# Kernel optimization log

Hardware: AMD Instinct MI355X
Metric: run time of the kernel (lower is better)

The kernel has to match this reference:

```python
import jax, jax.numpy as jnp
import numpy as np

N_NODES = 100000
N_EDGES = 1600000
C = 64       # in_channels == filters
K = 3        # Chebyshev order
EPS = 1e-5   # InstanceNorm eps


def setup_inputs() -> dict:
    key = jax.random.key(0)
    ks = jax.random.split(key, 8)
    x = jax.random.normal(ks[0], (N_NODES, C), dtype=jnp.float32)
    edge_index = jax.random.randint(ks[1], (2, N_EDGES), 0, N_NODES, dtype=jnp.int64)
    scale = 1.0 / np.sqrt(C)
    W1 = jax.random.normal(ks[2], (K, C, C), dtype=jnp.float32) * scale
    b1 = jnp.zeros((C,), dtype=jnp.float32)
    W2 = jax.random.normal(ks[3], (K, C, C), dtype=jnp.float32) * scale
    b2 = jnp.zeros((C,), dtype=jnp.float32)
    return {"x": x, "edge_index": edge_index, "W1": W1, "b1": b1, "W2": W2, "b2": b2}


def _cheb_conv(x, src, dst, w_edge, W, b, n):
    # PyG ChebConv, norm='sym', lambda_max=2: L_hat = -D^{-1/2} A D^{-1/2}
    def prop(h):  # h: [N, C] -> L_hat @ h via gather -> weight -> scatter-add
        return jax.ops.segment_sum(w_edge[:, None] * h[src], dst, num_segments=n)
    Tx0 = x
    Tx1 = prop(x)
    Tx2 = 2.0 * prop(Tx1) - Tx0
    return Tx0 @ W[0] + Tx1 @ W[1] + Tx2 @ W[2] + b


def _instance_norm(h):
    # PyG InstanceNorm (single graph, affine=False): normalize over nodes per channel
    m = h.mean(axis=0, keepdims=True)
    v = h.var(axis=0, keepdims=True)
    return (h - m) * jax.lax.rsqrt(v + EPS)


def reference(x, edge_index, W1, b1, W2, b2):
    n = x.shape[0]
    src, dst = edge_index[0], edge_index[1]
    ones = jnp.ones((src.shape[0],), dtype=x.dtype)
    deg = jax.ops.segment_sum(ones, dst, num_segments=n)
    safe = jnp.where(deg > 0, deg, 1.0)
    dinv = jnp.where(deg > 0, jax.lax.rsqrt(safe), 0.0)
    w_edge = -dinv[src] * dinv[dst]  # scaled-Laplacian edge weights
    h = _instance_norm(jax.nn.relu(_cheb_conv(x, src, dst, w_edge, W1, b1, n)))
    h = _instance_norm(jax.nn.relu(_cheb_conv(h, src, dst, w_edge, W2, b2, n)))
    return h
```

## Files before the change

### kernel.cpp

```cpp
#include <hip/hip_runtime.h>
#include <hip/hip_fp16.h>

#define NCH 64
#define EPS 1e-5f
#define SBANKS 32
#define BSHIFT 8
#define NHIST 256
#define BINCAP 6400
#define PADRES 2048
#define RSHIFT 14
#define SRCMASK 0x1FFFFu
#define QW_SCALE 32767.0f
#define QW_INV (1.0f/32767.0f)

typedef _Float16 f16x8 __attribute__((ext_vector_type(8)));
typedef float f32x4 __attribute__((ext_vector_type(4)));

__global__ __launch_bounds__(256) void k_front(const float* __restrict__ x, __half* __restrict__ xh,
                                               int castTotal, int castB,
                                               const float* __restrict__ W1, _Float16* __restrict__ Wb1,
                                               const float* __restrict__ W2, _Float16* __restrict__ Wb2,
                                               const int* __restrict__ dst, int* __restrict__ cnt,
                                               int E, int per, int nbuck) {
    int bid = blockIdx.x;
    if (bid < castB) {
        int i = (bid * 256 + threadIdx.x) * 4;
        if (i < castTotal) {
            float4 f = *(const float4*)(x + i);
            __half2* o = (__half2*)(xh + i);
            o[0] = __floats2half2_rn(f.x, f.y);
            o[1] = __floats2half2_rn(f.z, f.w);
        }
        return;
    }
    if (bid < castB + 96) {
        int wb = bid - castB;
        const float* W = (wb < 48) ? W1 : W2;
        _Float16* Wb = (wb < 48) ? Wb1 : Wb2;
        int idx = (wb % 48) * 256 + threadIdx.x;
        int j = idx & 7;
        int lane = (idx >> 3) & 63;
        int tk = idx >> 9;
        int tile = tk / 6, kk = tk % 6;
        int k = kk * 32 + (lane >> 4) * 8 + j;
        int n = tile * 16 + (lane & 15);
        Wb[idx] = (_Float16)W[k * 64 + n];
        return;
    }
    __shared__ int lh[512];
    int hb = bid - castB - 96;
    for (int t = threadIdx.x; t < nbuck; t += 256) lh[t] = 0;
    __syncthreads();
    int lo = hb * per, hi = min(E, lo + per);
    for (int e = lo + threadIdx.x; e < hi; e += 256)
        atomicAdd(&lh[dst[e] >> BSHIFT], 1);
    __syncthreads();
    for (int t = threadIdx.x; t < nbuck; t += 256)
        if (lh[t]) atomicAdd(&cnt[t], lh[t]);
}

__global__ void k_bscan(const int* __restrict__ cnt, int* __restrict__ gbase,
                        int* __restrict__ gcur, int nbuck, int E) {
    __shared__ int s[512];
    int t = threadIdx.x;
    int v = (t < nbuck) ? cnt[t] : 0;
    s[t] = v;
    __syncthreads();
    for (int off = 1; off < 512; off <<= 1) {
        int add = (t >= off) ? s[t - off] : 0;
        __syncthreads();
        s[t] += add;
        __syncthreads();
    }
    if (t < nbuck) { int ex = s[t] - v; gbase[t] = ex; gcur[t] = ex; }
    if (t == 0) gbase[nbuck] = E;
}

__global__ __launch_bounds__(256) void k_bin(const int* __restrict__ src,
                                             const int* __restrict__ dst,
                                             int* __restrict__ gcur,
                                             int2* __restrict__ binned, int E, int per, int nbuck) {
    __shared__ int lh[512];
    __shared__ int lsc[512];
    __shared__ int lbase[512];
    __shared__ int lcur[512];
    __shared__ int2 sedge[BINCAP];
    int t = threadIdx.x;
    for (int i = t; i < 512; i += 256) lh[i] = 0;
    __syncthreads();
    int lo = blockIdx.x * per, hi = min(E, lo + per);
    for (int e = lo + t; e < hi; e += 256)
        atomicAdd(&lh[dst[e] >> BSHIFT], 1);
    __syncthreads();
    int v0 = lh[t], v1 = lh[t + 256];
    lsc[t] = v0; lsc[t + 256] = v1;
    __syncthreads();
    for (int off = 1; off < 512; off <<= 1) {
        int a0 = (t >= off) ? lsc[t - off] : 0;
        int a1 = (t + 256 >= off) ? lsc[t + 256 - off] : 0;
        __syncthreads();
        lsc[t] += a0; lsc[t + 256] += a1;
        __syncthreads();
    }
    lsc[t] -= v0; lsc[t + 256] -= v1;
    if (t < nbuck && v0) lbase[t] = atomicAdd(&gcur[t], v0);
    if (t + 256 < nbuck && v1) lbase[t + 256] = atomicAdd(&gcur[t + 256], v1);
    lcur[t] = lsc[t]; lcur[t + 256] = lsc[t + 256];
    __syncthreads();
    for (int e = lo + t; e < hi; e += 256) {
        int d = dst[e];
        int b = d >> BSHIFT;
        int pos = atomicAdd(&lcur[b], 1);
        sedge[pos] = make_int2(src[e], d);
    }
    __syncthreads();
    int cntE = hi - lo;
    for (int i = t; i < cntE; i += 256) {
        int2 sd = sedge[i];
        int b = sd.y >> BSHIFT;
        binned[lbase[b] + (i - lsc[b])] = sd;
    }
}

__global__ __launch_bounds__(256) void k_bucket(const int2* __restrict__ binned,
                                                const int* __restrict__ gbase,
                                                float* __restrict__ dinv,
                                                int2* __restrict__ rowinfo,
                                                unsigned int* __restrict__ csr, int N, int nbuck) {
    __shared__ int hist8[256 * 8];
    __shared__ int cur8[256 * 8];
    __shared__ int ldeg[256];
    __shared__ int ltmp[256];
    int b = blockIdx.x;
    int t = threadIdx.x;
    int nodeLo = b << BSHIFT;
    int nHere = min(256, N - nodeLo);
    int e0 = gbase[b], e1 = gbase[b + 1];
    int pb = (gbase[b] + b * PADRES + 7) & ~7;
    for (int i = t; i < 256 * 8; i += 256) hist8[i] = 0;
    __syncthreads();
    for (int e = e0 + t; e < e1; e += 256) {
        int2 sd = binned[e];
        atomicAdd(&hist8[((sd.y - nodeLo) << 3) + (sd.x >> RSHIFT)], 1);
    }
    __syncthreads();
    int c[8], deg = 0;
#pragma unroll
    for (int r = 0; r < 8; r++) { c[r] = hist8[(t << 3) + r]; deg += c[r]; }
    int pdeg = (deg + 7) & ~7;
    ldeg[t] = deg;
    if (t < nHere) dinv[nodeLo + t] = (deg > 0) ? rsqrtf((float)deg) : 0.0f;
    ltmp[t] = pdeg;
    __syncthreads();
    for (int off = 1; off < 256; off <<= 1) {
        int add = (t >= off) ? ltmp[t - off] : 0;
        __syncthreads();
        ltmp[t] += add;
        __syncthreads();
    }
    int lstart = ltmp[t] - pdeg;
    if (t < nHere) rowinfo[nodeLo + t] = make_int2(pb + lstart, pdeg);
    int run = lstart;
#pragma unroll
    for (int r = 0; r < 8; r++) { cur8[(t << 3) + r] = run; run += c[r]; }
    __syncthreads();
    for (int e = e0 + t; e < e1; e += 256) {
        int2 sd = binned[e];
        int dl = sd.y - nodeLo;
        int pos = atomicAdd(&cur8[(dl << 3) + (sd.x >> RSHIFT)], 1);
        unsigned int dd = (unsigned int)min(ldeg[dl], 32767);
        csr[pb + pos] = (unsigned int)sd.x | (dd << 17);
    }
    __syncthreads();
    if (t < nHere) {
        int d = ldeg[t];
        int pd = (d + 7) & ~7;
        if (pd > d) {
            unsigned int fill = (d > 0) ? (csr[pb + lstart] & SRCMASK) : 0u;
            for (int i = d; i < pd; i++) csr[pb + lstart + i] = fill;
        }
    }
}

__global__ void k_weights(unsigned int* __restrict__ csr, const float* __restrict__ dinv, int PE) {
    int e = blockIdx.x * blockDim.x + threadIdx.x;
    if (e < PE) {
        unsigned int v = csr[e];
        unsigned int d = v >> 17;
        if (d == 0) return;
        unsigned int s = v & SRCMASK;
        float aw = dinv[s] * rsqrtf((float)d);
        unsigned int qw = (unsigned int)(aw * QW_SCALE + 0.5f);
        csr[e] = s | (qw << 17);
    }
}


#define GATH(A0,A1,A2,A3,A4,A5,A6,A7, C0, C1) \
    A0 = *(const uint4*)(hb + (size_t)(C0.x & SRCMASK) * NCH); \
    A1 = *(const uint4*)(hb + (size_t)(C0.y & SRCMASK) * NCH); \
    A2 = *(const uint4*)(hb + (size_t)(C0.z & SRCMASK) * NCH); \
    A3 = *(const uint4*)(hb + (size_t)(C0.w & SRCMASK) * NCH); \
    A4 = *(const uint4*)(hb + (size_t)(C1.x & SRCMASK) * NCH); \
    A5 = *(const uint4*)(hb + (size_t)(C1.y & SRCMASK) * NCH); \
    A6 = *(const uint4*)(hb + (size_t)(C1.z & SRCMASK) * NCH); \
    A7 = *(const uint4*)(hb + (size_t)(C1.w & SRCMASK) * NCH);

#define FMA1(A, W) { \
    float2 f; \
    f = __half22float2(*(const __half2*)&A.x); acc[0] = fmaf(W, f.x, acc[0]); acc[1] = fmaf(W, f.y, acc[1]); \
    f = __half22float2(*(const __half2*)&A.y); acc[2] = fmaf(W, f.x, acc[2]); acc[3] = fmaf(W, f.y, acc[3]); \
    f = __half22float2(*(const __half2*)&A.z); acc[4] = fmaf(W, f.x, acc[4]); acc[5] = fmaf(W, f.y, acc[5]); \
    f = __half22float2(*(const __half2*)&A.w); acc[6] = fmaf(W, f.x, acc[6]); acc[7] = fmaf(W, f.y, acc[7]); }

#define FMA8(A0,A1,A2,A3,A4,A5,A6,A7, C0, C1) { \
    float w0 = -(float)(C0.x >> 17) * QW_INV; \
    float w1 = -(float)(C0.y >> 17) * QW_INV; \
    float w2 = -(float)(C0.z >> 17) * QW_INV; \
    float w3 = -(float)(C0.w >> 17) * QW_INV; \
    float w4 = -(float)(C1.x >> 17) * QW_INV; \
    float w5 = -(float)(C1.y >> 17) * QW_INV; \
    float w6 = -(float)(C1.z >> 17) * QW_INV; \
    float w7 = -(float)(C1.w >> 17) * QW_INV; \
    sw += ((w0 + w1) + (w2 + w3)) + ((w4 + w5) + (w6 + w7)); \
    FMA1(A0, w0) FMA1(A1, w1) FMA1(A2, w2) FMA1(A3, w3) \
    FMA1(A4, w4) FMA1(A5, w5) FMA1(A6, w6) FMA1(A7, w7) }

__global__ __launch_bounds__(256) void k_prop(const __half* __restrict__ h,
                                              const int2* __restrict__ rowinfo,
                                              const unsigned int* __restrict__ csr,
                                              const __half* __restrict__ tx0,
                                              __half* __restrict__ y, int N,
                                              const float* __restrict__ gstats,
                                              const float* __restrict__ tstats) {
    int lane = threadIdx.x & 63;
    int wv = (blockIdx.x * 256 + threadIdx.x) >> 6;
    int g = lane >> 3, li = lane & 7;
    int node = wv * 8 + g;
    int e = 0, eN = 0;
    if (node < N) {
        int2 info = rowinfo[node];
        e = info.x;
        eN = info.x + info.y;
    }
    float acc[8] = {0.f, 0.f, 0.f, 0.f, 0.f, 0.f, 0.f, 0.f};
    float sw = 0.0f;
    const __half* hb = h + li * 8;
    uint4 c0, c1, d0, d1;
    uint4 a0, a1, a2, a3, a4, a5, a6, a7;
    uint4 b0, b1, b2, b3, b4, b5, b6, b7;
    if (e < eN) {
        c0 = *(const uint4*)(csr + e);
        c1 = *(const uint4*)(csr + e + 4);
        int en = (e + 8 < eN) ? e + 8 : e;
        d0 = *(const uint4*)(csr + en);
        d1 = *(const uint4*)(csr + en + 4);
        GATH(a0, a1, a2, a3, a4, a5, a6, a7, c0, c1);
    }
    while (e + 8 < eN) {
        GATH(b0, b1, b2, b3, b4, b5, b6, b7, d0, d1);
        bool hasT = (e + 16 < eN);
        int enT = hasT ? e + 16 : e;
        uint4 t0 = *(const uint4*)(csr + enT);
        uint4 t1 = *(const uint4*)(csr + enT + 4);
        FMA8(a0, a1, a2, a3, a4, a5, a6, a7, c0, c1);
        if (hasT) { GATH(a0, a1, a2, a3, a4, a5, a6, a7, t0, t1); }
        int enD = (e + 24 < eN) ? e + 24 : e;
        uint4 u0 = *(const uint4*)(csr + enD);
        uint4 u1 = *(const uint4*)(csr + enD + 4);
        FMA8(b0, b1, b2, b3, b4, b5, b6, b7, d0, d1);
        c0 = t0; c1 = t1; d0 = u0; d1 = u1;
        e += 16;
    }
    if (e < eN) { FMA8(a0, a1, a2, a3, a4, a5, a6, a7, c0, c1); }
    if (node >= N) return;
    if (gstats != nullptr) {
        float4 m0 = *(const float4*)(gstats + li * 8);
        float4 m1 = *(const float4*)(gstats + li * 8 + 4);
        float4 r0 = *(const float4*)(gstats + 64 + li * 8);
        float4 r1 = *(const float4*)(gstats + 64 + li * 8 + 4);
        acc[0] = r0.x * (acc[0] - m0.x * sw);
        acc[1] = r0.y * (acc[1] - m0.y * sw);
        acc[2] = r0.z * (acc[2] - m0.z * sw);
        acc[3] = r0.w * (acc[3] - m0.w * sw);
        acc[4] = r1.x * (acc[4] - m1.x * sw);
        acc[5] = r1.y * (acc[5] - m1.y * sw);
        acc[6] = r1.z * (acc[6] - m1.z * sw);
        acc[7] = r1.w * (acc[7] - m1.w * sw);
    }
    if (tx0 != nullptr) {
        uint4 tq = *(const uint4*)(tx0 + (size_t)node * NCH + li * 8);
        float tv[8];
        float2 f;
        f = __half22float2(*(__half2*)&tq.x); tv[0] = f.x; tv[1] = f.y;
        f = __half22float2(*(__half2*)&tq.y); tv[2] = f.x; tv[3] = f.y;
        f = __half22float2(*(__half2*)&tq.z); tv[4] = f.x; tv[5] = f.y;
        f = __half22float2(*(__half2*)&tq.w); tv[6] = f.x; tv[7] = f.y;
        if (tstats != nullptr) {
            float4 m0 = *(const float4*)(tstats + li * 8);
            float4 m1 = *(const float4*)(tstats + li * 8 + 4);
            float4 r0 = *(const float4*)(tstats + 64 + li * 8);
            float4 r1 = *(const float4*)(tstats + 64 + li * 8 + 4);
            tv[0] = (tv[0] - m0.x) * r0.x; tv[1] = (tv[1] - m0.y) * r0.y;
            tv[2] = (tv[2] - m0.z) * r0.z; tv[3] = (tv[3] - m0.w) * r0.w;
            tv[4] = (tv[4] - m1.x) * r1.x; tv[5] = (tv[5] - m1.y) * r1.y;
            tv[6] = (tv[6] - m1.z) * r1.z; tv[7] = (tv[7] - m1.w) * r1.w;
        }
#pragma unroll
        for (int j = 0; j < 8; j++) acc[j] = 2.0f * acc[j] - tv[j];
    }
    uint4 o;
    __half2 hh;
    hh = __floats2half2_rn(acc[0], acc[1]); o.x = *(unsigned int*)&hh;
    hh = __floats2half2_rn(acc[2], acc[3]); o.y = *(unsigned int*)&hh;
    hh = __floats2half2_rn(acc[4], acc[5]); o.z = *(unsigned int*)&hh;
    hh = __floats2half2_rn(acc[6], acc[7]); o.w = *(unsigned int*)&hh;
    *(uint4*)(y + (size_t)node * NCH + li * 8) = o;
}

template <typename TOUT>
__global__ __launch_bounds__(256) void k_dmm(const __half* __restrict__ tx0,
                                             const __half* __restrict__ tx1,
                                             const __half* __restrict__ tx2,
                                             const _Float16* __restrict__ Wb,
                                             const float* __restrict__ b,
                                             TOUT* __restrict__ out,
                                             float* __restrict__ statsP, int N,
                                             const float* __restrict__ tstats) {
    __shared__ float sred[64];
    __shared__ float sq[64];
    int t = threadIdx.x;
    int w = t >> 6;
    int lane = t & 63;
    if (t < 64) { sred[t] = 0.f; sq[t] = 0.f; }
    __syncthreads();

    int nb16 = blockIdx.x * 64 + w * 16;
    int m = lane & 15, q = lane >> 4;
    int row = nb16 + m;
    int rowC = (row < N) ? row : 0;
    const __half* base0 = tx0 + (size_t)rowC * NCH;
    const __half* base1 = tx1 + (size_t)rowC * NCH;
    const __half* base2 = tx2 + (size_t)rowC * NCH;

    f32x4 acc[4];
#pragma unroll
    for (int tile = 0; tile < 4; tile++) acc[tile] = (f32x4){0.f, 0.f, 0.f, 0.f};

#pragma unroll
    for (int kk = 0; kk < 6; kk++) {
        const __half* ap = (kk < 2 ? base0 : (kk < 4 ? base1 : base2)) + (kk & 1) * 32 + q * 8;
        f16x8 a = *(const f16x8*)ap;
        if (kk < 2 && tstats != nullptr) {
            int cbase = (kk & 1) * 32 + q * 8;
#pragma unroll
            for (int j = 0; j < 8; j++) {
                float v = (float)a[j];
                a[j] = (_Float16)((v - tstats[cbase + j]) * tstats[64 + cbase + j]);
            }
        }
#pragma unroll
        for (int tile = 0; tile < 4; tile++) {
            f16x8 bf = *(const f16x8*)(Wb + ((size_t)(tile * 6 + kk) * 64 + lane) * 8);
            acc[tile] = __builtin_amdgcn_mfma_f32_16x16x32_f16(a, bf, acc[tile], 0, 0, 0);
        }
    }

#pragma unroll
    for (int tile = 0; tile < 4; tile++) {
        int ch = tile * 16 + m;
        float bb = b[ch];
        float s = 0.f, qq = 0.f;
#pragma unroll
        for (int r = 0; r < 4; r++) {
            int node = nb16 + q * 4 + r;
            float v = fmaxf(acc[tile][r] + bb, 0.f);
            if (node < N) {
                out[(size_t)node * NCH + ch] = (TOUT)v;
                s += v;
                qq = fmaf(v, v, qq);
            }
        }
        s += __shfl_xor(s, 16, 64);  s += __shfl_xor(s, 32, 64);
        qq += __shfl_xor(qq, 16, 64); qq += __shfl_xor(qq, 32, 64);
        if (q == 0) { atomicAdd(&sred[ch], s); atomicAdd(&sq[ch], qq); }
    }
    __syncthreads();
    if (t < 64) {
        int bank = blockIdx.x & (SBANKS - 1);
        atomicAdd(&statsP[bank * 128 + t], sred[t]);
        atomicAdd(&statsP[bank * 128 + 64 + t], sq[t]);
    }
}

__global__ void k_final(float* __restrict__ statsP, float invN) {
    int c = threadIdx.x;
    float S = 0.f, Q = 0.f;
    for (int k = 0; k < SBANKS; k++) {
        S += statsP[k * 128 + c];
        Q += statsP[k * 128 + 64 + c];
    }
    float m = S * invN;
    float var = Q * invN - m * m;
    statsP[SBANKS * 128 + c] = m;
    statsP[SBANKS * 128 + 64 + c] = rsqrtf(var + EPS);
}

__global__ void k_norm_hf(const __half* __restrict__ a, float* __restrict__ o,
                          const float* __restrict__ statsP, int total) {
    int i = blockIdx.x * blockDim.x + threadIdx.x;
    if (i >= total) return;
    int lane = i & 63;
    o[i] = (__half2float(a[i]) - statsP[SBANKS * 128 + lane]) * statsP[SBANKS * 128 + 64 + lane];
}

extern "C" void kernel_launch(void* const* d_in, const int* in_sizes, int n_in,
                              void* d_out, int out_size, void* d_ws, size_t ws_size,
                              hipStream_t stream) {
    const float* x  = (const float*)d_in[0];
    const int*   ei = (const int*)d_in[1];
    const float* W1 = (const float*)d_in[2];
    const float* b1 = (const float*)d_in[3];
    const float* W2 = (const float*)d_in[4];
    const float* b2 = (const float*)d_in[5];
    float* out = (float*)d_out;

    const int N = in_sizes[0] / NCH;
    const int E = in_sizes[1] / 2;
    const int* src = ei;
    const int* dst = ei + E;
    const int nbuck = (N + 255) >> BSHIFT;
    const int PE = E + nbuck * PADRES + 8;

    char* p = (char*)d_ws;
    auto alloc = [&](size_t bytes) {
        void* r = (void*)p;
        p += ((bytes + 255) / 256) * 256;
        return r;
    };
    float*  dinv     = (float*)alloc((size_t)131072 * 4);
    int2*   rowinfo  = (int2*)alloc((size_t)N * 8);
    unsigned int* csr = (unsigned int*)alloc((size_t)PE * 4);
    __half* xh       = (__half*)alloc((size_t)N * NCH * 2);
    __half* Tx1      = (__half*)alloc((size_t)N * NCH * 2);
    __half* Tx2      = (__half*)alloc((size_t)N * NCH * 2);
    __half* A        = (__half*)alloc((size_t)N * NCH * 2);
    __half* A2       = (__half*)alloc((size_t)N * NCH * 2);
    _Float16* Wb1    = (_Float16*)alloc(12288 * 2);
    _Float16* Wb2    = (_Float16*)alloc(12288 * 2);
    int*    gbase    = (int*)alloc((size_t)(nbuck + 1) * 4);
    int*    gcur     = (int*)alloc((size_t)nbuck * 4);
    const int statsFloats = SBANKS * 128 + 128;
    int*    cnt      = (int*)alloc((size_t)nbuck * 4 + (size_t)2 * statsFloats * 4);
    float*  stats1   = (float*)(cnt + nbuck);
    float*  stats2   = stats1 + statsFloats;
    const float* nrm1 = stats1 + SBANKS * 128;

    int2* binned = (int2*)Tx1;

    hipMemsetAsync(cnt, 0, (size_t)nbuck * 4 + (size_t)2 * statsFloats * 4, stream);

    const int TB = 256;
    int nbin = (E + BINCAP - 1) / BINCAP;
    if (nbin < 256) nbin = 256;
    const int perBin = (E + nbin - 1) / nbin;
    const int perH = (E + NHIST - 1) / NHIST;
    const int castTotal = N * NCH;
    const int castB = (castTotal / 4 + TB - 1) / TB;
    k_front<<<castB + 96 + NHIST, TB, 0, stream>>>(x, xh, castTotal, castB,
                                                   W1, Wb1, W2, Wb2,
                                                   dst, cnt, E, perH, nbuck);
    k_bscan<<<1, 512, 0, stream>>>(cnt, gbase, gcur, nbuck, E);
    k_bin<<<nbin, TB, 0, stream>>>(src, dst, gcur, binned, E, perBin, nbuck);
    k_bucket<<<nbuck, TB, 0, stream>>>(binned, gbase, dinv, rowinfo, csr, N, nbuck);
    k_weights<<<(PE + TB - 1) / TB, TB, 0, stream>>>(csr, dinv, PE);

    const int propWaves = (N + 7) / 8;
    const int propBlocks = (propWaves + 3) / 4;
    const int dmmBlocks = (N + 63) / 64;
    const int normBlocks = (N * NCH + TB - 1) / TB;
    const float invN = 1.0f / (float)N;

    k_prop<<<propBlocks, TB, 0, stream>>>(xh, rowinfo, csr, nullptr, Tx1, N, nullptr, nullptr);
    k_prop<<<propBlocks, TB, 0, stream>>>(Tx1, rowinfo, csr, xh, Tx2, N, nullptr, nullptr);
    k_dmm<__half><<<dmmBlocks, TB, 0, stream>>>(xh, Tx1, Tx2, Wb1, b1, A, stats1, N, nullptr);
    k_final<<<1, 64, 0, stream>>>(stats1, invN);

    k_prop<<<propBlocks, TB, 0, stream>>>(A, rowinfo, csr, nullptr, Tx1, N, nrm1, nullptr);
    k_prop<<<propBlocks, TB, 0, stream>>>(Tx1, rowinfo, csr, A, Tx2, N, nullptr, nrm1);
    k_dmm<__half><<<dmmBlocks, TB, 0, stream>>>(A, Tx1, Tx2, Wb2, b2, A2, stats2, N, nrm1);
    k_final<<<1, 64, 0, stream>>>(stats2, invN);
    k_norm_hf<<<normBlocks, TB, 0, stream>>>(A2, out, stats2, N * NCH);
}
```

Before: 341.7 us.

## Sort nodes by padded degree class to balance SpMM waves, simplify gather loop

Adds a degree-class histogram in k_bucket and a new k_perm kernel that builds a permutation grouping nodes by padded degree. Each k_prop wave now takes nodes from this permutation, so the 8 nodes sharing a wave have similar edge counts and less lane divergence. The software-pipelined double-buffered gather loop is replaced by a simple one-chunk-per-iteration loop. Costs are an extra kernel launch, an indirect perm load, scattered output writes and less memory-level parallelism per wave.

```diff
diff --git a/kernel.cpp b/kernel.cpp
--- a/kernel.cpp
+++ b/kernel.cpp
@@ -126,11 +126,13 @@
                                                 const int* __restrict__ gbase,
                                                 float* __restrict__ dinv,
                                                 int2* __restrict__ rowinfo,
-                                                unsigned int* __restrict__ csr, int N, int nbuck) {
+                                                unsigned int* __restrict__ csr,
+                                                int* __restrict__ pcnt, int N, int nbuck) {
     __shared__ int hist8[256 * 8];
     __shared__ int cur8[256 * 8];
     __shared__ int ldeg[256];
     __shared__ int ltmp[256];
+    __shared__ int lcls[16];
     int b = blockIdx.x;
     int t = threadIdx.x;
     int nodeLo = b << BSHIFT;
@@ -138,6 +140,7 @@
     int e0 = gbase[b], e1 = gbase[b + 1];
     int pb = (gbase[b] + b * PADRES + 7) & ~7;
     for (int i = t; i < 256 * 8; i += 256) hist8[i] = 0;
+    if (t < 16) lcls[t] = 0;
     __syncthreads();
     for (int e = e0 + t; e < e1; e += 256) {
         int2 sd = binned[e];
@@ -149,7 +152,11 @@
     for (int r = 0; r < 8; r++) { c[r] = hist8[(t << 3) + r]; deg += c[r]; }
     int pdeg = (deg + 7) & ~7;
     ldeg[t] = deg;
-    if (t < nHere) dinv[nodeLo + t] = (deg > 0) ? rsqrtf((float)deg) : 0.0f;
+    if (t < nHere) {
+        dinv[nodeLo + t] = (deg > 0) ? rsqrtf((float)deg) : 0.0f;
+        int cls = pdeg >> 3; if (cls > 15) cls = 15;
+        atomicAdd(&lcls[cls], 1);
+    }
     ltmp[t] = pdeg;
     __syncthreads();
     for (int off = 1; off < 256; off <<= 1) {
@@ -179,6 +186,37 @@
             unsigned int fill = (d > 0) ? (csr[pb + lstart] & SRCMASK) : 0u;
             for (int i = d; i < pd; i++) csr[pb + lstart + i] = fill;
         }
+    }
+    if (t < 16 && lcls[t]) atomicAdd(&pcnt[t], lcls[t]);
+}
+
+__global__ __launch_bounds__(256) void k_perm(const int2* __restrict__ rowinfo,
+                                              const int* __restrict__ pcnt,
+                                              int* __restrict__ pcur,
+                                              int* __restrict__ perm, int N) {
+    __shared__ int sbase[16];
+    __shared__ int lc[16];
+    __shared__ int lbase[16];
+    __shared__ int lcur[16];
+    int t = threadIdx.x;
+    int node = blockIdx.x * 256 + t;
+    if (t == 0) {
+        int run = 0;
+        for (int i = 0; i < 16; i++) { sbase[i] = run; run += pcnt[i]; }
+    }
+    if (t < 16) { lc[t] = 0; lcur[t] = 0; }
+    __syncthreads();
+    int cls = 0;
+    if (node < N) {
+        cls = rowinfo[node].y >> 3; if (cls > 15) cls = 15;
+        atomicAdd(&lc[cls], 1);
+    }
+    __syncthreads();
+    if (t < 16 && lc[t]) lbase[t] = sbase[t] + atomicAdd(&pcur[t], lc[t]);
+    __syncthreads();
+    if (node < N) {
+        int r = atomicAdd(&lcur[cls], 1);
+        perm[lbase[cls] + r] = node;
     }
 }
 
@@ -229,6 +267,7 @@
 __global__ __launch_bounds__(256) void k_prop(const __half* __restrict__ h,
                                               const int2* __restrict__ rowinfo,
                                               const unsigned int* __restrict__ csr,
+                                              const int* __restrict__ perm,
                                               const __half* __restrict__ tx0,
                                               __half* __restrict__ y, int N,
                                               const float* __restrict__ gstats,
@@ -236,44 +275,26 @@
     int lane = threadIdx.x & 63;
     int wv = (blockIdx.x * 256 + threadIdx.x) >> 6;
     int g = lane >> 3, li = lane & 7;
-    int node = wv * 8 + g;
-    int e = 0, eN = 0;
-    if (node < N) {
+    int idx = wv * 8 + g;
+    int node = 0;
+    int e = 0, e1 = 0;
+    if (idx < N) {
+        node = perm[idx];
         int2 info = rowinfo[node];
         e = info.x;
-        eN = info.x + info.y;
+        e1 = info.x + info.y;
     }
     float acc[8] = {0.f, 0.f, 0.f, 0.f, 0.f, 0.f, 0.f, 0.f};
     float sw = 0.0f;
     const __half* hb = h + li * 8;
-    uint4 c0, c1, d0, d1;
-    uint4 a0, a1, a2, a3, a4, a5, a6, a7;
-    uint4 b0, b1, b2, b3, b4, b5, b6, b7;
-    if (e < eN) {
-        c0 = *(const uint4*)(csr + e);
-        c1 = *(const uint4*)(csr + e + 4);
-        int en = (e + 8 < eN) ? e + 8 : e;
-        d0 = *(const uint4*)(csr + en);
-        d1 = *(const uint4*)(csr + en + 4);
+    for (; e < e1; e += 8) {
+        uint4 c0 = *(const uint4*)(csr + e);
+        uint4 c1 = *(const uint4*)(csr + e + 4);
+        uint4 a0, a1, a2, a3, a4, a5, a6, a7;
         GATH(a0, a1, a2, a3, a4, a5, a6, a7, c0, c1);
-    }
-    while (e + 8 < eN) {
-        GATH(b0, b1, b2, b3, b4, b5, b6, b7, d0, d1);
-        bool hasT = (e + 16 < eN);
-        int enT = hasT ? e + 16 : e;
-        uint4 t0 = *(const uint4*)(csr + enT);
-        uint4 t1 = *(const uint4*)(csr + enT + 4);
         FMA8(a0, a1, a2, a3, a4, a5, a6, a7, c0, c1);
-        if (hasT) { GATH(a0, a1, a2, a3, a4, a5, a6, a7, t0, t1); }
-        int enD = (e + 24 < eN) ? e + 24 : e;
-        uint4 u0 = *(const uint4*)(csr + enD);
-        uint4 u1 = *(const uint4*)(csr + enD + 4);
-        FMA8(b0, b1, b2, b3, b4, b5, b6, b7, d0, d1);
-        c0 = t0; c1 = t1; d0 = u0; d1 = u1;
-        e += 16;
-    }
-    if (e < eN) { FMA8(a0, a1, a2, a3, a4, a5, a6, a7, c0, c1); }
-    if (node >= N) return;
+    }
+    if (idx >= N) return;
     if (gstats != nullptr) {
         float4 m0 = *(const float4*)(gstats + li * 8);
         float4 m1 = *(const float4*)(gstats + li * 8 + 4);
@@ -450,15 +471,18 @@
     _Float16* Wb2    = (_Float16*)alloc(12288 * 2);
     int*    gbase    = (int*)alloc((size_t)(nbuck + 1) * 4);
     int*    gcur     = (int*)alloc((size_t)nbuck * 4);
+    int*    perm     = (int*)alloc((size_t)N * 4);
     const int statsFloats = SBANKS * 128 + 128;
-    int*    cnt      = (int*)alloc((size_t)nbuck * 4 + (size_t)2 * statsFloats * 4);
-    float*  stats1   = (float*)(cnt + nbuck);
+    int*    cnt      = (int*)alloc((size_t)nbuck * 4 + 32 * 4 + (size_t)2 * statsFloats * 4);
+    int*    pcnt     = cnt + nbuck;
+    int*    pcur     = pcnt + 16;
+    float*  stats1   = (float*)(pcur + 16);
     float*  stats2   = stats1 + statsFloats;
     const float* nrm1 = stats1 + SBANKS * 128;
 
     int2* binned = (int2*)Tx1;
 
-    hipMemsetAsync(cnt, 0, (size_t)nbuck * 4 + (size_t)2 * statsFloats * 4, stream);
+    hipMemsetAsync(cnt, 0, (size_t)nbuck * 4 + 32 * 4 + (size_t)2 * statsFloats * 4, stream);
 
     const int TB = 256;
     int nbin = (E + BINCAP - 1) / BINCAP;
@@ -472,7 +496,8 @@
                                                    dst, cnt, E, perH, nbuck);
     k_bscan<<<1, 512, 0, stream>>>(cnt, gbase, gcur, nbuck, E);
     k_bin<<<nbin, TB, 0, stream>>>(src, dst, gcur, binned, E, perBin, nbuck);
-    k_bucket<<<nbuck, TB, 0, stream>>>(binned, gbase, dinv, rowinfo, csr, N, nbuck);
+    k_bucket<<<nbuck, TB, 0, stream>>>(binned, gbase, dinv, rowinfo, csr, pcnt, N, nbuck);
+    k_perm<<<nbuck, TB, 0, stream>>>(rowinfo, pcnt, pcur, perm, N);
     k_weights<<<(PE + TB - 1) / TB, TB, 0, stream>>>(csr, dinv, PE);
 
     const int propWaves = (N + 7) / 8;
@@ -481,13 +506,13 @@
     const int normBlocks = (N * NCH + TB - 1) / TB;
     const float invN = 1.0f / (float)N;
 
-    k_prop<<<propBlocks, TB, 0, stream>>>(xh, rowinfo, csr, nullptr, Tx1, N, nullptr, nullptr);
-    k_prop<<<propBlocks, TB, 0, stream>>>(Tx1, rowinfo, csr, xh, Tx2, N, nullptr, nullptr);
+    k_prop<<<propBlocks, TB, 0, stream>>>(xh, rowinfo, csr, perm, nullptr, Tx1, N, nullptr, nullptr);
+    k_prop<<<propBlocks, TB, 0, stream>>>(Tx1, rowinfo, csr, perm, xh, Tx2, N, nullptr, nullptr);
     k_dmm<__half><<<dmmBlocks, TB, 0, stream>>>(xh, Tx1, Tx2, Wb1, b1, A, stats1, N, nullptr);
     k_final<<<1, 64, 0, stream>>>(stats1, invN);
 
-    k_prop<<<propBlocks, TB, 0, stream>>>(A, rowinfo, csr, nullptr, Tx1, N, nrm1, nullptr);
-    k_prop<<<propBlocks, TB, 0, stream>>>(Tx1, rowinfo, csr, A, Tx2, N, nullptr, nrm1);
+    k_prop<<<propBlocks, TB, 0, stream>>>(A, rowinfo, csr, perm, nullptr, Tx1, N, nrm1, nullptr);
+    k_prop<<<propBlocks, TB, 0, stream>>>(Tx1, rowinfo, csr, perm, A, Tx2, N, nullptr, nrm1);
     k_dmm<__half><<<dmmBlocks, TB, 0, stream>>>(A, Tx1, Tx2, Wb2, b2, A2, stats2, N, nrm1);
     k_final<<<1, 64, 0, stream>>>(stats2, invN);
     k_norm_hf<<<normBlocks, TB, 0, stream>>>(A2, out, stats2, N * NCH);
```

Measured after the change: 354.3 us. +3.7%, slower.
